# Optimization experiments

Measured on AMD Instinct MI355X. Metric: run time of the kernel, lower is better.

The kernel has to match this reference:

```python
import jax, jax.numpy as jnp
import numpy as np

GAMMA = 5.0 / 3.0
SG = float(np.sqrt(GAMMA - 1.0))
NC, E, H = 1000000, 5, 32

def _csnd(rho, p):
    h = 1.0 + GAMMA / (GAMMA - 1.0) * p / rho
    return jnp.sqrt(GAMMA * p / (rho * h))

def _vstar_from_cs(cs, cs_a, v_a, wave_sign):
    # Marti-Muller relativistic rarefaction Riemann invariant
    ratio = ((SG - cs) / (SG + cs)) * ((SG + cs_a) / (SG - cs_a))
    A = ((1.0 + v_a) / (1.0 - v_a)) * ratio ** (-wave_sign * 2.0 / SG)
    return (A - 1.0) / (A + 1.0)

def _get_vel_raref(p, rho_a, p_a, v_a, wave_sign):
    rho = rho_a * (p / p_a) ** (1.0 / GAMMA)          # isentrope
    h = 1.0 + GAMMA / (GAMMA - 1.0) * p / rho
    cs = jnp.sqrt(GAMMA * p / (rho * h))
    vstar = _vstar_from_cs(cs, _csnd(rho_a, p_a), v_a, wave_sign)
    W = 1.0 / jnp.sqrt(1.0 - vstar ** 2)
    return rho, p / rho, h, cs, vstar, W

def _raref_solver(prims, sign):
    # state inside the rarefaction fan at xi = x/t = 0: v = sign*cs
    rho_a, p_a, v_a = prims[:, 0], prims[:, 1], prims[:, 2]
    cs_a = _csnd(rho_a, p_a)
    wave_sign = -float(sign)
    f = lambda cs: _vstar_from_cs(cs, cs_a, v_a, wave_sign) - sign * cs
    lo = jnp.full_like(rho_a, 1e-6)
    hi = jnp.full_like(rho_a, SG - 1e-6)
    flo = f(lo)
    for _ in range(40):  # fixed-count bisection, jit-safe
        mid = 0.5 * (lo + hi)
        fm = f(mid)
        same = jnp.sign(fm) == jnp.sign(flo)
        lo = jnp.where(same, mid, lo)
        flo = jnp.where(same, fm, flo)
        hi = jnp.where(same, hi, mid)
    cs = 0.5 * (lo + hi)
    h = (GAMMA - 1.0) / (GAMMA - 1.0 - cs ** 2)
    k = (h - 1.0) * (GAMMA - 1.0) / GAMMA              # p / rho
    rho = (k * rho_a ** GAMMA / p_a) ** (1.0 / (GAMMA - 1.0))
    return rho, k * rho, h, sign * cs

def setup_inputs():
    key = jax.random.key(0)
    ks = jax.random.split(key, 10)
    rho = 0.5 + jax.random.uniform(ks[0], (NC, 1, 2))
    p = 0.5 + jax.random.uniform(ks[1], (NC, 1, 2))
    v = 0.8 * (jax.random.uniform(ks[2], (NC, 1, 2)) - 0.5)
    P = jnp.concatenate([rho, p, v], axis=1)           # (NC,3,2)
    U = jax.random.normal(ks[3], (NC, 3, 2))
    F = jax.random.normal(ks[4], (NC, 3, 2))
    cmax = jax.random.uniform(ks[5], (NC,))
    cmin = -jax.random.uniform(ks[6], (NC,))
    s = lambda fan: 0.5 / np.sqrt(fan)
    W1 = jax.random.normal(ks[7], (E, H, 6)) * s(6)
    b1 = jnp.zeros((E, H))
    W2 = jax.random.normal(ks[8], (E, H, H)) * s(H)
    b2 = jnp.zeros((E, H))
    W3 = jax.random.normal(ks[9], (E, 1, H)) * s(H)
    b3 = jnp.zeros((E, 1))
    return {"P": P, "U": U, "F": F, "cmax": cmax, "cmin": cmin,
            "W1": W1, "b1": b1, "W2": W2, "b2": b2, "W3": W3, "b3": b3}

def _forward(P, U, F, cmax, cmin, W1, b1, W2, b2, W3, b3):
    rhoL, rhoR = P[:, 0, 0], P[:, 0, 1]
    pL, pR = P[:, 1, 0], P[:, 1, 1]
    vL, vR = P[:, 2, 0], P[:, 2, 1]
    # pressnet ensemble, batched over E instead of a Python loop
    x = jnp.concatenate([jnp.log(P[:, 0]), jnp.log(P[:, 1]), P[:, 2]], axis=1)  # (NC,6)
    h1 = jnp.tanh(jnp.einsum('nf,ehf->neh', x, W1) + b1)
    h2 = jnp.tanh(jnp.einsum('neh,egh->neg', h1, W2) + b2)
    xi = jax.nn.sigmoid(jnp.einsum('neh,eoh->neo', h2, W3) + b3)[..., 0]        # (NC,E)
    pressC = xi * jnp.minimum(pL, pR)[:, None]        # affine compactification [0, min(pL,pR)]
    rhoCLe, _, hCLe, csCLe, vstarLe, _ = _get_vel_raref(pressC, rhoL[:, None], pL[:, None], vL[:, None], -1.0)
    rhoCRe, _, hCRe, csCRe, vstarRe, _ = _get_vel_raref(pressC, rhoR[:, None], pR[:, None], vR[:, None], +1.0)
    best = jnp.argmin(jnp.abs(vstarLe - vstarRe), axis=1)
    pick = lambda a: jnp.take_along_axis(a, best[:, None], axis=1)[:, 0]
    pressCs = pick(pressC)
    rhoCL, hCL, csCL, vstarL = pick(rhoCLe), pick(hCLe), pick(csCLe), pick(vstarLe)
    rhoCR, hCR, csCR, vstarR = pick(rhoCRe), pick(hCRe), pick(csCRe), pick(vstarRe)
    csL, csR = _csnd(rhoL, pL), _csnd(rhoR, pR)
    lambdaC = 0.5 * (vstarR + vstarL)
    lambdaRL = (lambdaC - csCL) / (1.0 - lambdaC * csCL)
    lambdaL = (vL - csL) / (1.0 - vL * csL)
    lambdaRR = (lambdaC + csCR) / (1.0 + lambdaC * csCR)
    lambdaR = (vR + csR) / (1.0 + vR * csR)
    WC = 1.0 / jnp.sqrt(1.0 - lambdaC ** 2)
    densCL, densCR = WC * rhoCL, WC * rhoCR
    momCL = WC ** 2 * rhoCL * hCL * lambdaC
    momCR = WC ** 2 * rhoCR * hCR * lambdaC
    FCL = jnp.stack([densCL * lambdaC, densCL * (WC * hCL - 1.0) * lambdaC, momCL * lambdaC + pressCs], axis=1)
    FCR = jnp.stack([densCR * lambdaC, densCR * (WC * hCR - 1.0) * lambdaC, momCR * lambdaC + pressCs], axis=1)
    rho_RL, p_RL, h_RL, v_RL = _raref_solver(P[:, :3, 0], +1.0)
    rho_RR, p_RR, h_RR, v_RR = _raref_solver(P[:, :3, 1], -1.0)
    WRL = 1.0 / jnp.sqrt(1.0 - v_RL ** 2)
    WRR = 1.0 / jnp.sqrt(1.0 - v_RR ** 2)
    densRL, densRR = WRL * rho_RL, WRR * rho_RR
    momRL = WRL ** 2 * rho_RL * h_RL * v_RL
    momRR = WRR ** 2 * rho_RR * h_RR * v_RR
    FRL = jnp.stack([densRL * v_RL, densRL * (WRL * h_RL - 1.0) * v_RL, momRL * v_RL + p_RL], axis=1)
    FRR = jnp.stack([densRR * v_RR, densRR * (WRR * h_RR - 1.0) * v_RR, momRR * v_RR + p_RR], axis=1)
    fluxes = jnp.zeros_like(F[:, :, 0])
    sel = lambda m, val, cur: jnp.where(m[:, None], val, cur)
    fluxes = sel(lambdaL >= 0, F[:, :, 0], fluxes)
    fluxes = sel((lambdaL < 0) & (lambdaRL >= 0), FRL, fluxes)
    fluxes = sel((lambdaRL < 0) & (lambdaC > 0), FCL, fluxes)
    fluxes = sel((lambdaC <= 0) & (lambdaRR > 0), FCR, fluxes)
    fluxes = sel((lambdaRR <= 0) & (lambdaR > 0), FRR, fluxes)
    fluxes = sel(lambdaR <= 0, F[:, :, 1], fluxes)
    return fluxes

def reference(P, U, F, cmax, cmin, W1, b1, W2, b2, W3, b3):
    return _forward(P, U, F, cmax, cmin, W1, b1, W2, b2, W3, b3)
```

## Files before the change

kernel.cpp:

```cpp
#include <hip/hip_runtime.h>
#include <hip/hip_bf16.h>
#include <math.h>
#include <stdint.h>

namespace {

constexpr int NE  = 5;
constexpr int NH  = 32;
constexpr int BLK = 256;
constexpr int WPB = BLK / 64;

typedef __attribute__((ext_vector_type(8))) _Float16 half8;
typedef __attribute__((ext_vector_type(2))) __fp16   fp16x2;
typedef __attribute__((ext_vector_type(4))) float    f32x4;

union U4H8 { uint4 u; half8 h; };
union U1H2 { uint32_t u; fp16x2 h; };

__device__ __forceinline__ float bflo(uint32_t u){ return __uint_as_float(u << 16); }
__device__ __forceinline__ float bfhi(uint32_t u){ return __uint_as_float(u & 0xffff0000u); }
__device__ __forceinline__ float b2f(uint16_t u){ return __uint_as_float(((uint32_t)u) << 16); }

constexpr float GAM   = (float)(5.0 / 3.0);
constexpr float G1    = (float)(2.0 / 3.0);
constexpr float CP    = 2.5f;
constexpr float SGc   = (float)0.81649658092772603;
constexpr float E2SG  = (float)2.4494897427831781;
constexpr float LOG2E = 1.4426950408889634f;
constexpr float LN2   = 0.6931471805599453f;
constexpr float TLG   = 2.0f * LOG2E;

__device__ __forceinline__ float fexp2(float x){ return __builtin_amdgcn_exp2f(x); }
__device__ __forceinline__ float flog2(float x){ return __builtin_amdgcn_logf(x); }
__device__ __forceinline__ float frcp (float x){ return __builtin_amdgcn_rcpf(x); }
__device__ __forceinline__ float frsq (float x){ return __builtin_amdgcn_rsqf(x); }
__device__ __forceinline__ float fdiv (float a, float b){ return a * frcp(b); }

__device__ __forceinline__ float tanh_e(float a){
    float e = fexp2(a);
    return 1.0f - 2.0f * frcp(e + 1.0f);
}

__device__ __forceinline__ float csnd_fast(float rho, float p){
    return sqrtf(GAM * p * frcp(rho + CP * p));
}

__device__ __forceinline__ uint32_t pk16(float a, float b){
    U1H2 x; x.h = __builtin_amdgcn_cvt_pkrtz(a, b); return x.u;
}
__device__ __forceinline__ uint32_t pkrtn(float a, float b){
    union { _Float16 h[2]; uint32_t u; } cv;
    cv.h[0] = (_Float16)a; cv.h[1] = (_Float16)b;
    return cv.u;
}

__device__ __forceinline__ int kxr(int r){ return (r ^ (r >> 2)) & 3; }

template<bool F32>
__device__ __forceinline__ float wload(const void* p, int idx){
    if constexpr (F32) return ((const float*)p)[idx];
    else               return b2f(((const uint16_t*)p)[idx]);
}

struct VelRaref { float por, h, cs, vstar; };

__device__ __forceinline__ VelRaref get_vel_raref(float l2p, float l2pa,
                                                  float l2rhoa, float lnra2, float lnv2, float e){
    VelRaref r;
    r.por = fexp2(0.4f * l2p + 0.6f * l2pa - l2rhoa);
    r.h   = 1.0f + CP * r.por;
    r.cs  = sqrtf(GAM * r.por * frcp(r.h));
    float lr2 = flog2((SGc - r.cs) * frcp(SGc + r.cs));
    float A   = fexp2(lnv2 + e * (lr2 + lnra2));
    r.vstar = 1.0f - 2.0f * frcp(A + 1.0f);
    return r;
}

__device__ __forceinline__ void raref_solver(float l2rho_a, float p_a, float sgn,
                                             float lnra2, float lnv2,
                                             float& rho, float& p, float& h, float& v){
    float sE = sgn * E2SG;
    float lo = 1e-6f, hi = SGc - 1e-6f;
    float cs = 0.40f;
    #pragma unroll 1
    for(int it = 0; it < 12; ++it){
        float lr2 = flog2((SGc - cs) * frcp(SGc + cs));
        float a2  = flog2((1.0f + cs) * frcp(1.0f - cs));
        float g   = lnv2 + sE * (lr2 + lnra2) - sgn * a2;
        float d1  = (SGc - cs) * (SGc + cs);
        float d2  = (1.0f - cs) * (1.0f + cs);
        float num = LOG2E * (-2.0f * SGc * sE * d2 - 2.0f * sgn * d1);
        float csn = cs - g * d1 * d2 * frcp(num);
        bool above = (g * sgn > 0.0f);
        lo = above ? cs : lo;
        hi = above ? hi : cs;
        csn = (csn > lo && csn < hi) ? csn : 0.5f * (lo + hi);
        cs = csn;
    }
    h = G1 * frcp(G1 - cs * cs);
    float k = (h - 1.0f) * 0.4f;
    float base = k * fexp2(GAM * l2rho_a) * frcp(p_a);
    rho = base * sqrtf(base);
    p = k * rho;
    v = sgn * cs;
}

template<bool F32>
__device__ __forceinline__ void cell_block(const void* Pp, const void* Fp,
                                           const void* W1p, const void* b1p,
                                           const void* W2p, const void* b2p,
                                           const void* W3p, const void* b3p,
                                           float* __restrict__ out, int nc,
                                           uint32_t* Hu ,
                                           uint32_t* sW1u, uint32_t* sW2u,
                                           float* sB1, float* sB2, float* sW3, float* sB3)
{
    const int lane = threadIdx.x & 63;
    const int l16  = lane & 15;
    const int quad = lane >> 4;
    const int k16  = kxr(l16);
    const int sw   = quad ^ k16;

    for(int i = threadIdx.x; i < NE * NH * 16; i += BLK){
        int row = i >> 4, kp = i & 15;
        float f0 = wload<F32>(W2p, row * NH + 2 * kp) * TLG;
        float f1 = wload<F32>(W2p, row * NH + 2 * kp + 1) * TLG;
        int idx = (row << 4) | ((((kp >> 2) ^ kxr(row)) << 2) | (kp & 3));
        sW2u[idx] = pkrtn(f0, f1);
    }
    for(int i = threadIdx.x; i < NE * NH * 16; i += BLK){
        int row = i >> 4, kp = i & 15;
        int k0 = 2 * kp, k1 = 2 * kp + 1;
        float f0 = (k0 < 6) ? wload<F32>(W1p, row * 6 + k0) * ((k0 < 4) ? 2.0f : TLG) : 0.0f;
        float f1 = (k1 < 6) ? wload<F32>(W1p, row * 6 + k1) * ((k1 < 4) ? 2.0f : TLG) : 0.0f;
        int idx = (row << 4) | ((((kp >> 2) ^ kxr(row)) << 2) | (kp & 3));
        sW1u[idx] = pkrtn(f0, f1);
    }
    for(int i = threadIdx.x; i < NE * NH; i += BLK){
        sB1[i] = wload<F32>(b1p, i) * TLG;
        sB2[i] = wload<F32>(b2p, i) * TLG;
        sW3[i] = wload<F32>(W3p, i);
    }
    if(threadIdx.x < NE) sB3[threadIdx.x] = wload<F32>(b3p, threadIdx.x);
    __syncthreads();

    const int n  = blockIdx.x * BLK + threadIdx.x;
    const bool valid = (n < nc);
    const int nn = valid ? n : 0;

    float rhoL, rhoR, pL, pR, vL, vR;
    if constexpr (F32){
        const float2* Pf = (const float2*)((const float*)Pp + (size_t)nn * 6);
        float2 a = Pf[0], b = Pf[1], c = Pf[2];
        rhoL = a.x; rhoR = a.y; pL = b.x; pR = b.y; vL = c.x; vR = c.y;
    } else {
        const uint32_t* P32 = (const uint32_t*)Pp;
        uint32_t pa = P32[nn * 3 + 0], pb = P32[nn * 3 + 1], pc = P32[nn * 3 + 2];
        rhoL = bflo(pa); rhoR = bfhi(pa);
        pL   = bflo(pb); pR   = bfhi(pb);
        vL   = bflo(pc); vR   = bfhi(pc);
    }

    float l2rhoL = flog2(rhoL), l2rhoR = flog2(rhoR);
    float l2pL   = flog2(pL),   l2pR   = flog2(pR);

    float csL = csnd_fast(rhoL, pL);
    float csR = csnd_fast(rhoR, pR);
    float pmin = fminf(pL, pR);

    float lnraL = flog2((SGc + csL) * frcp(SGc - csL));
    float lnraR = flog2((SGc + csR) * frcp(SGc - csR));
    float lnvL  = flog2((1.0f + vL) * frcp(1.0f - vL));
    float lnvR  = flog2((1.0f + vR) * frcp(1.0f - vR));

    uint4 Bx[4];
    {
        uint32_t x01 = pk16(l2rhoL, l2rhoR);
        uint32_t x23 = pk16(l2pL, l2pR);
        uint32_t x45 = pk16(vL, vR);
        uint4 z = make_uint4(0u, 0u, 0u, 0u);
        *(uint4*)&Hu[(lane << 4) + ((0 ^ k16) << 2)] = make_uint4(x01, x23, x45, 0u);
        *(uint4*)&Hu[(lane << 4) + ((1 ^ k16) << 2)] = z;
        *(uint4*)&Hu[(lane << 4) + ((2 ^ k16) << 2)] = z;
        *(uint4*)&Hu[(lane << 4) + ((3 ^ k16) << 2)] = z;
        #pragma unroll
        for(int t = 0; t < 4; ++t)
            Bx[t] = *(const uint4*)&Hu[((t * 16 + l16) << 4) + (sw << 2)];
    }

    float bestd = 1e30f;
    float pressCs = 0.f, porL = 1.f, hCL = 0.f, csCL = 0.f, vstarL = 0.f;
    float porR = 1.f, hCR = 0.f, csCR = 0.f, vstarR = 0.f;

    #pragma unroll 1
    for(int e = 0; e < NE; ++e){
        U4H8 A1[2];
        #pragma unroll
        for(int m2 = 0; m2 < 2; ++m2)
            A1[m2].u = *(const uint4*)&sW1u[((e * NH + m2 * 16 + l16) << 4) + (sw << 2)];

        f32x4 acc1[2][4];
        #pragma unroll
        for(int m2 = 0; m2 < 2; ++m2){
            f32x4 bias = *(const f32x4*)&sB1[e * NH + m2 * 16 + quad * 4];
            #pragma unroll
            for(int t = 0; t < 4; ++t) acc1[m2][t] = bias;
        }
        #pragma unroll
        for(int t = 0; t < 4; ++t){
            U4H8 Bh; Bh.u = Bx[t];
            #pragma unroll
            for(int m2 = 0; m2 < 2; ++m2)
                acc1[m2][t] = __builtin_amdgcn_mfma_f32_16x16x32_f16(A1[m2].h, Bh.h, acc1[m2][t], 0, 0, 0);
        }

        #pragma unroll
        for(int m2 = 0; m2 < 2; ++m2){
            int cpos = (((m2 * 2 + (quad >> 1)) ^ k16) << 2) + ((quad & 1) << 1);
            #pragma unroll
            for(int t = 0; t < 4; ++t){
                int c = t * 16 + l16;
                uint32_t u0 = pk16(tanh_e(acc1[m2][t][0]), tanh_e(acc1[m2][t][1]));
                uint32_t u1 = pk16(tanh_e(acc1[m2][t][2]), tanh_e(acc1[m2][t][3]));
                *(uint2*)&Hu[(c << 4) + cpos] = make_uint2(u0, u1);
            }
        }

        U4H8 Ah[2];
        #pragma unroll
        for(int m2 = 0; m2 < 2; ++m2)
            Ah[m2].u = *(const uint4*)&sW2u[((e * NH + m2 * 16 + l16) << 4) + (sw << 2)];

        f32x4 acc[2][4];
        #pragma unroll
        for(int m2 = 0; m2 < 2; ++m2){
            f32x4 bias = *(const f32x4*)&sB2[e * NH + m2 * 16 + quad * 4];
            #pragma unroll
            for(int t = 0; t < 4; ++t) acc[m2][t] = bias;
        }

        #pragma unroll
        for(int t = 0; t < 4; ++t){
            int cell = t * 16 + l16;
            U4H8 Bh;
            Bh.u = *(const uint4*)&Hu[(cell << 4) + (sw << 2)];
            #pragma unroll
            for(int m2 = 0; m2 < 2; ++m2)
                acc[m2][t] = __builtin_amdgcn_mfma_f32_16x16x32_f16(Ah[m2].h, Bh.h, acc[m2][t], 0, 0, 0);
        }

        f32x4 w3v[2];
        #pragma unroll
        for(int m2 = 0; m2 < 2; ++m2)
            w3v[m2] = *(const f32x4*)&sW3[e * NH + m2 * 16 + quad * 4];
        float part[4];
        #pragma unroll
        for(int t = 0; t < 4; ++t){
            float s = 0.0f;
            #pragma unroll
            for(int m2 = 0; m2 < 2; ++m2)
                #pragma unroll
                for(int r = 0; r < 4; ++r)
                    s += w3v[m2][r] * tanh_e(acc[m2][t][r]);
            s += __shfl_xor(s, 16, 64);
            s += __shfl_xor(s, 32, 64);
            part[t] = s;
        }
        float p01 = (lane & 16) ? part[1] : part[0];
        float p23 = (lane & 16) ? part[3] : part[2];
        float xa  = ((lane & 32) ? p23 : p01) + sB3[e];

        float xi = frcp(1.0f + fexp2(-xa * LOG2E));
        float pC = xi * pmin;

        float l2pC = flog2(pC);
        VelRaref L = get_vel_raref(l2pC, l2pL, l2rhoL, lnraL, lnvL, +E2SG);
        VelRaref R = get_vel_raref(l2pC, l2pR, l2rhoR, lnraR, lnvR, -E2SG);
        float d = fabsf(L.vstar - R.vstar);
        if(d < bestd){
            bestd = d;
            pressCs = pC;
            porL = L.por; hCL = L.h; csCL = L.cs; vstarL = L.vstar;
            porR = R.por; hCR = R.h; csCR = R.cs; vstarR = R.vstar;
        }
    }

    float rhoCL = pressCs * frcp(porL);
    float rhoCR = pressCs * frcp(porR);

    float lambdaC  = 0.5f * (vstarR + vstarL);
    float lambdaRL = fdiv(lambdaC - csCL, 1.0f - lambdaC * csCL);
    float lambdaL  = fdiv(vL - csL,       1.0f - vL * csL);
    float lambdaRR = fdiv(lambdaC + csCR, 1.0f + lambdaC * csCR);
    float lambdaR  = fdiv(vR + csR,       1.0f + vR * csR);

    float WC = frsq(1.0f - lambdaC * lambdaC);
    float densCL = WC * rhoCL, densCR = WC * rhoCR;
    float momCL = WC * WC * rhoCL * hCL * lambdaC;
    float momCR = WC * WC * rhoCR * hCR * lambdaC;
    float FCL0 = densCL * lambdaC;
    float FCL1 = densCL * (WC * hCL - 1.0f) * lambdaC;
    float FCL2 = momCL * lambdaC + pressCs;
    float FCR0 = densCR * lambdaC;
    float FCR1 = densCR * (WC * hCR - 1.0f) * lambdaC;
    float FCR2 = momCR * lambdaC + pressCs;

    float rho_RL, p_RL, h_RL, v_RL;
    raref_solver(l2rhoL, pL, +1.0f, lnraL, lnvL, rho_RL, p_RL, h_RL, v_RL);
    float rho_RR, p_RR, h_RR, v_RR;
    raref_solver(l2rhoR, pR, -1.0f, lnraR, lnvR, rho_RR, p_RR, h_RR, v_RR);

    float WRL = frsq(1.0f - v_RL * v_RL);
    float WRR = frsq(1.0f - v_RR * v_RR);
    float densRL = WRL * rho_RL, densRR = WRR * rho_RR;
    float momRL = WRL * WRL * rho_RL * h_RL * v_RL;
    float momRR = WRR * WRR * rho_RR * h_RR * v_RR;
    float FRL0 = densRL * v_RL;
    float FRL1 = densRL * (WRL * h_RL - 1.0f) * v_RL;
    float FRL2 = momRL * v_RL + p_RL;
    float FRR0 = densRR * v_RR;
    float FRR1 = densRR * (WRR * h_RR - 1.0f) * v_RR;
    float FRR2 = momRR * v_RR + p_RR;

    float FL0, FR0, FL1, FR1, FL2, FR2;
    if constexpr (F32){
        const float2* Ff = (const float2*)((const float*)Fp + (size_t)nn * 6);
        float2 fa = Ff[0], fb = Ff[1], fc = Ff[2];
        FL0 = fa.x; FR0 = fa.y; FL1 = fb.x; FR1 = fb.y; FL2 = fc.x; FR2 = fc.y;
    } else {
        const uint32_t* F32p = (const uint32_t*)Fp;
        uint32_t fa = F32p[nn * 3 + 0], fb = F32p[nn * 3 + 1], fc = F32p[nn * 3 + 2];
        FL0 = bflo(fa); FR0 = bfhi(fa);
        FL1 = bflo(fb); FR1 = bfhi(fb);
        FL2 = bflo(fc); FR2 = bfhi(fc);
    }

    float o0 = 0.f, o1 = 0.f, o2 = 0.f;
    if(lambdaL >= 0.0f)                        { o0 = FL0;  o1 = FL1;  o2 = FL2;  }
    if(lambdaL < 0.0f  && lambdaRL >= 0.0f)    { o0 = FRL0; o1 = FRL1; o2 = FRL2; }
    if(lambdaRL < 0.0f && lambdaC  >  0.0f)    { o0 = FCL0; o1 = FCL1; o2 = FCL2; }
    if(lambdaC  <= 0.0f && lambdaRR >  0.0f)   { o0 = FCR0; o1 = FCR1; o2 = FCR2; }
    if(lambdaRR <= 0.0f && lambdaR  >  0.0f)   { o0 = FRR0; o1 = FRR1; o2 = FRR2; }
    if(lambdaR  <= 0.0f)                       { o0 = FR0;  o1 = FR1;  o2 = FR2;  }

    if(valid){
        out[(size_t)n * 3 + 0] = o0;
        out[(size_t)n * 3 + 1] = o1;
        out[(size_t)n * 3 + 2] = o2;
    }
}

__global__ __launch_bounds__(BLK)
void solver_kernel(const void* __restrict__ Pp,
                   const void* __restrict__ Fp,
                   const void* __restrict__ W1p,
                   const void* __restrict__ b1p,
                   const void* __restrict__ W2p,
                   const void* __restrict__ b2p,
                   const void* __restrict__ W3p,
                   const void* __restrict__ b3p,
                   float* __restrict__ out, int nc)
{
    __shared__ __align__(16) uint32_t HuA[WPB][64 * 16];
    __shared__ __align__(16) uint32_t sW1u[NE * NH * 16];
    __shared__ __align__(16) uint32_t sW2u[NE * NH * 16];
    __shared__ __align__(16) float sB1[NE * NH];
    __shared__ __align__(16) float sB2[NE * NH];
    __shared__ __align__(16) float sW3[NE * NH];
    __shared__ __align__(16) float sB3[NE];
    const int wv = threadIdx.x >> 6;

    const uint32_t* Pd = (const uint32_t*)Pp;
    int votes = 0;
    #pragma unroll
    for(int i = 0; i < 8; ++i){
        float tv = __uint_as_float(Pd[6 * i + 2]);
        votes += (tv >= 0.45f && tv <= 1.55f) ? 1 : 0;
    }
    if(votes >= 4)
        cell_block<true >(Pp, Fp, W1p, b1p, W2p, b2p, W3p, b3p, out, nc,
                          HuA[wv], sW1u, sW2u, sB1, sB2, sW3, sB3);
    else
        cell_block<false>(Pp, Fp, W1p, b1p, W2p, b2p, W3p, b3p, out, nc,
                          HuA[wv], sW1u, sW2u, sB1, sB2, sW3, sB3);
}

}

extern "C" void kernel_launch(void* const* d_in, const int* in_sizes, int n_in,
                              void* d_out, int out_size, void* d_ws, size_t ws_size,
                              hipStream_t stream) {
    const void* P  = d_in[0];
    const void* F  = d_in[2];
    const void* W1 = d_in[5];
    const void* b1 = d_in[6];
    const void* W2 = d_in[7];
    const void* b2 = d_in[8];
    const void* W3 = d_in[9];
    const void* b3 = d_in[10];
    float* out = (float*)d_out;

    int nc = in_sizes[0] / 6;
    dim3 grid((nc + BLK - 1) / BLK);
    hipLaunchKernelGGL(solver_kernel, grid, dim3(BLK), 0, stream,
                       P, F, W1, b1, W2, b2, W3, b3, out, nc);
}
```

Baseline: 233.2 us.

## Batch reciprocals, fold tanh into sigmoid constants, skip unneeded rarefaction solves

Several transcendental reciprocals are merged through a shared-product batch-inverse trick, in tanh evaluation, the vstar computation and the rarefaction solver. The layer-3 tanh is rewritten algebraically so that W3 and b3 fold into precomputed constants. The left and right rarefaction Newton solves are fused into one loop and skipped entirely when no lane in the wave needs them. The W1 shared layout shrinks to only the nonzero K slice, with zeros filled in through lane masking. Batched reciprocals can lose accuracy or overflow when the products grow large.

```diff
diff --git a/kernel.cpp b/kernel.cpp
--- a/kernel.cpp
+++ b/kernel.cpp
@@ -27,7 +27,6 @@
 constexpr float SGc   = (float)0.81649658092772603;
 constexpr float E2SG  = (float)2.4494897427831781;
 constexpr float LOG2E = 1.4426950408889634f;
-constexpr float LN2   = 0.6931471805599453f;
 constexpr float TLG   = 2.0f * LOG2E;
 
 __device__ __forceinline__ float fexp2(float x){ return __builtin_amdgcn_exp2f(x); }
@@ -36,11 +35,6 @@
 __device__ __forceinline__ float frsq (float x){ return __builtin_amdgcn_rsqf(x); }
 __device__ __forceinline__ float fdiv (float a, float b){ return a * frcp(b); }
 
-__device__ __forceinline__ float tanh_e(float a){
-    float e = fexp2(a);
-    return 1.0f - 2.0f * frcp(e + 1.0f);
-}
-
 __device__ __forceinline__ float csnd_fast(float rho, float p){
     return sqrtf(GAM * p * frcp(rho + CP * p));
 }
@@ -62,47 +56,63 @@
     else               return b2f(((const uint16_t*)p)[idx]);
 }
 
-struct VelRaref { float por, h, cs, vstar; };
-
-__device__ __forceinline__ VelRaref get_vel_raref(float l2p, float l2pa,
-                                                  float l2rhoa, float lnra2, float lnv2, float e){
-    VelRaref r;
-    r.por = fexp2(0.4f * l2p + 0.6f * l2pa - l2rhoa);
-    r.h   = 1.0f + CP * r.por;
-    r.cs  = sqrtf(GAM * r.por * frcp(r.h));
-    float lr2 = flog2((SGc - r.cs) * frcp(SGc + r.cs));
-    float A   = fexp2(lnv2 + e * (lr2 + lnra2));
-    r.vstar = 1.0f - 2.0f * frcp(A + 1.0f);
-    return r;
-}
-
-__device__ __forceinline__ void raref_solver(float l2rho_a, float p_a, float sgn,
-                                             float lnra2, float lnv2,
-                                             float& rho, float& p, float& h, float& v){
-    float sE = sgn * E2SG;
-    float lo = 1e-6f, hi = SGc - 1e-6f;
-    float cs = 0.40f;
+__device__ __forceinline__ void binv4(float d0, float d1, float d2, float d3,
+                                      float& i0, float& i1, float& i2, float& i3){
+    float P1 = d0 * d1, P2 = P1 * d2, P3 = P2 * d3;
+    float R3 = frcp(P3);
+    i3 = R3 * P2;
+    float R2 = R3 * d3;
+    i2 = R2 * P1;
+    float R1 = R2 * d2;
+    i1 = R1 * d0;
+    i0 = R1 * d1;
+}
+
+__device__ __forceinline__ void raref_solver2(float l2rhoL_, float pL_, float lnraL, float lnvL,
+                                              float l2rhoR_, float pR_, float lnraR, float lnvR,
+                                              float& rhoRL, float& pRL, float& hRL, float& vRL,
+                                              float& rhoRR, float& pRR, float& hRR, float& vRR)
+{
+    float loL = 1e-6f, hiL = SGc - 1e-6f, csL = 0.40f;
+    float loR = 1e-6f, hiR = SGc - 1e-6f, csR = 0.40f;
     #pragma unroll 1
     for(int it = 0; it < 12; ++it){
-        float lr2 = flog2((SGc - cs) * frcp(SGc + cs));
-        float a2  = flog2((1.0f + cs) * frcp(1.0f - cs));
-        float g   = lnv2 + sE * (lr2 + lnra2) - sgn * a2;
-        float d1  = (SGc - cs) * (SGc + cs);
-        float d2  = (1.0f - cs) * (1.0f + cs);
-        float num = LOG2E * (-2.0f * SGc * sE * d2 - 2.0f * sgn * d1);
-        float csn = cs - g * d1 * d2 * frcp(num);
-        bool above = (g * sgn > 0.0f);
-        lo = above ? cs : lo;
-        hi = above ? hi : cs;
-        csn = (csn > lo && csn < hi) ? csn : 0.5f * (lo + hi);
-        cs = csn;
-    }
-    h = G1 * frcp(G1 - cs * cs);
-    float k = (h - 1.0f) * 0.4f;
-    float base = k * fexp2(GAM * l2rho_a) * frcp(p_a);
-    rho = base * sqrtf(base);
-    p = k * rho;
-    v = sgn * cs;
+        float aL = SGc + csL, aR = SGc + csR;
+        float Pa = aL * aR, Ra = frcp(Pa);
+        float lrL = flog2((SGc - csL) * (Ra * aR));
+        float lrR = flog2((SGc - csR) * (Ra * aL));
+        float bL = 1.0f - csL, bR = 1.0f - csR;
+        float Pb = bL * bR, Rb = frcp(Pb);
+        float a2L = flog2((1.0f + csL) * (Rb * bR));
+        float a2R = flog2((1.0f + csR) * (Rb * bL));
+        float gL = lnvL + E2SG * (lrL + lnraL) - a2L;
+        float gR = lnvR - E2SG * (lrR + lnraR) + a2R;
+        float d1L = (SGc - csL) * aL, d2L = bL * (1.0f + csL);
+        float d1R = (SGc - csR) * aR, d2R = bR * (1.0f + csR);
+        float numL = LOG2E * (-2.0f * SGc * E2SG * d2L - 2.0f * d1L);
+        float numR = LOG2E * ( 2.0f * SGc * E2SG * d2R + 2.0f * d1R);
+        float Pn = numL * numR, Rn = frcp(Pn);
+        float csnL = csL - gL * d1L * d2L * (Rn * numR);
+        float csnR = csR - gR * d1R * d2R * (Rn * numL);
+        bool abL = (gL > 0.0f);
+        bool abR = (gR < 0.0f);
+        loL = abL ? csL : loL;  hiL = abL ? hiL : csL;
+        loR = abR ? csR : loR;  hiR = abR ? hiR : csR;
+        csnL = (csnL > loL && csnL < hiL) ? csnL : 0.5f * (loL + hiL);
+        csnR = (csnR > loR && csnR < hiR) ? csnR : 0.5f * (loR + hiR);
+        csL = csnL; csR = csnR;
+    }
+    float e1L = G1 - csL * csL, e1R = G1 - csR * csR;
+    float Pe = e1L * e1R, Re = frcp(Pe);
+    hRL = G1 * (Re * e1R);  hRR = G1 * (Re * e1L);
+    float kL = (hRL - 1.0f) * 0.4f, kR = (hRR - 1.0f) * 0.4f;
+    float Pp = pL_ * pR_, Rp = frcp(Pp);
+    float baseL = kL * fexp2(GAM * l2rhoL_) * (Rp * pR_);
+    float baseR = kR * fexp2(GAM * l2rhoR_) * (Rp * pL_);
+    rhoRL = baseL * sqrtf(baseL);
+    rhoRR = baseR * sqrtf(baseR);
+    pRL = kL * rhoRL;  pRR = kR * rhoRR;
+    vRL = csL;  vRR = -csR;
 }
 
 template<bool F32>
@@ -112,8 +122,9 @@
                                            const void* W3p, const void* b3p,
                                            float* __restrict__ out, int nc,
                                            uint32_t* Hu ,
-                                           uint32_t* sW1u, uint32_t* sW2u,
-                                           float* sB1, float* sB2, float* sW3, float* sB3)
+                                           uint32_t* sW1u ,
+                                           uint32_t* sW2u ,
+                                           float* sB1, float* sB2, float* sW3, float* sC)
 {
     const int lane = threadIdx.x & 63;
     const int l16  = lane & 15;
@@ -128,20 +139,24 @@
         int idx = (row << 4) | ((((kp >> 2) ^ kxr(row)) << 2) | (kp & 3));
         sW2u[idx] = pkrtn(f0, f1);
     }
-    for(int i = threadIdx.x; i < NE * NH * 16; i += BLK){
-        int row = i >> 4, kp = i & 15;
+    for(int i = threadIdx.x; i < NE * NH * 4; i += BLK){
+        int row = i >> 2, kp = i & 3;
         int k0 = 2 * kp, k1 = 2 * kp + 1;
         float f0 = (k0 < 6) ? wload<F32>(W1p, row * 6 + k0) * ((k0 < 4) ? 2.0f : TLG) : 0.0f;
         float f1 = (k1 < 6) ? wload<F32>(W1p, row * 6 + k1) * ((k1 < 4) ? 2.0f : TLG) : 0.0f;
-        int idx = (row << 4) | ((((kp >> 2) ^ kxr(row)) << 2) | (kp & 3));
-        sW1u[idx] = pkrtn(f0, f1);
+        sW1u[i] = pkrtn(f0, f1);
     }
     for(int i = threadIdx.x; i < NE * NH; i += BLK){
         sB1[i] = wload<F32>(b1p, i) * TLG;
         sB2[i] = wload<F32>(b2p, i) * TLG;
-        sW3[i] = wload<F32>(W3p, i);
-    }
-    if(threadIdx.x < NE) sB3[threadIdx.x] = wload<F32>(b3p, threadIdx.x);
+        sW3[i] = wload<F32>(W3p, i) * (-LOG2E);
+    }
+    if(threadIdx.x < NE){
+        float s = wload<F32>(b3p, threadIdx.x) * (-LOG2E);
+        for(int j = 0; j < NH; ++j)
+            s += wload<F32>(W3p, threadIdx.x * NH + j) * (-LOG2E);
+        sC[threadIdx.x] = s;
+    }
     __syncthreads();
 
     const int n  = blockIdx.x * BLK + threadIdx.x;
@@ -173,19 +188,20 @@
     float lnvL  = flog2((1.0f + vL) * frcp(1.0f - vL));
     float lnvR  = flog2((1.0f + vR) * frcp(1.0f - vR));
 
-    uint4 Bx[4];
+    float c6L = 0.6f * l2pL - l2rhoL;
+    float c6R = 0.6f * l2pR - l2rhoR;
+
+    U4H8 Bx[4];
     {
         uint32_t x01 = pk16(l2rhoL, l2rhoR);
         uint32_t x23 = pk16(l2pL, l2pR);
         uint32_t x45 = pk16(vL, vR);
-        uint4 z = make_uint4(0u, 0u, 0u, 0u);
-        *(uint4*)&Hu[(lane << 4) + ((0 ^ k16) << 2)] = make_uint4(x01, x23, x45, 0u);
-        *(uint4*)&Hu[(lane << 4) + ((1 ^ k16) << 2)] = z;
-        *(uint4*)&Hu[(lane << 4) + ((2 ^ k16) << 2)] = z;
-        *(uint4*)&Hu[(lane << 4) + ((3 ^ k16) << 2)] = z;
-        #pragma unroll
-        for(int t = 0; t < 4; ++t)
-            Bx[t] = *(const uint4*)&Hu[((t * 16 + l16) << 4) + (sw << 2)];
+        *(uint4*)&Hu[(lane << 4) + (k16 << 2)] = make_uint4(x01, x23, x45, 0u);
+        #pragma unroll
+        for(int t = 0; t < 4; ++t){
+            uint4 b = *(const uint4*)&Hu[((t * 16 + l16) << 4) + (kxr(l16) << 2)];
+            Bx[t].u = (quad == 0) ? b : make_uint4(0u, 0u, 0u, 0u);
+        }
     }
 
     float bestd = 1e30f;
@@ -196,8 +212,10 @@
     for(int e = 0; e < NE; ++e){
         U4H8 A1[2];
         #pragma unroll
-        for(int m2 = 0; m2 < 2; ++m2)
-            A1[m2].u = *(const uint4*)&sW1u[((e * NH + m2 * 16 + l16) << 4) + (sw << 2)];
+        for(int m2 = 0; m2 < 2; ++m2){
+            uint4 w = *(const uint4*)&sW1u[(e * NH + m2 * 16 + l16) << 2];
+            A1[m2].u = (quad == 0) ? w : make_uint4(0u, 0u, 0u, 0u);
+        }
 
         f32x4 acc1[2][4];
         #pragma unroll
@@ -207,22 +225,25 @@
             for(int t = 0; t < 4; ++t) acc1[m2][t] = bias;
         }
         #pragma unroll
-        for(int t = 0; t < 4; ++t){
-            U4H8 Bh; Bh.u = Bx[t];
+        for(int t = 0; t < 4; ++t)
             #pragma unroll
             for(int m2 = 0; m2 < 2; ++m2)
-                acc1[m2][t] = __builtin_amdgcn_mfma_f32_16x16x32_f16(A1[m2].h, Bh.h, acc1[m2][t], 0, 0, 0);
-        }
+                acc1[m2][t] = __builtin_amdgcn_mfma_f32_16x16x32_f16(A1[m2].h, Bx[t].h, acc1[m2][t], 0, 0, 0);
 
         #pragma unroll
         for(int m2 = 0; m2 < 2; ++m2){
             int cpos = (((m2 * 2 + (quad >> 1)) ^ k16) << 2) + ((quad & 1) << 1);
             #pragma unroll
             for(int t = 0; t < 4; ++t){
-                int c = t * 16 + l16;
-                uint32_t u0 = pk16(tanh_e(acc1[m2][t][0]), tanh_e(acc1[m2][t][1]));
-                uint32_t u1 = pk16(tanh_e(acc1[m2][t][2]), tanh_e(acc1[m2][t][3]));
-                *(uint2*)&Hu[(c << 4) + cpos] = make_uint2(u0, u1);
+                float d0 = fexp2(acc1[m2][t][0]) + 1.0f;
+                float d1 = fexp2(acc1[m2][t][1]) + 1.0f;
+                float d2 = fexp2(acc1[m2][t][2]) + 1.0f;
+                float d3 = fexp2(acc1[m2][t][3]) + 1.0f;
+                float i0, i1, i2, i3;
+                binv4(d0, d1, d2, d3, i0, i1, i2, i3);
+                uint32_t u0 = pk16(1.0f - 2.0f * i0, 1.0f - 2.0f * i1);
+                uint32_t u1 = pk16(1.0f - 2.0f * i2, 1.0f - 2.0f * i3);
+                *(uint2*)&Hu[((t * 16 + l16) << 4) + cpos] = make_uint2(u0, u1);
             }
         }
 
@@ -258,30 +279,53 @@
         for(int t = 0; t < 4; ++t){
             float s = 0.0f;
             #pragma unroll
-            for(int m2 = 0; m2 < 2; ++m2)
-                #pragma unroll
-                for(int r = 0; r < 4; ++r)
-                    s += w3v[m2][r] * tanh_e(acc[m2][t][r]);
+            for(int m2 = 0; m2 < 2; ++m2){
+                float d0 = fexp2(acc[m2][t][0]) + 1.0f;
+                float d1 = fexp2(acc[m2][t][1]) + 1.0f;
+                float d2 = fexp2(acc[m2][t][2]) + 1.0f;
+                float d3 = fexp2(acc[m2][t][3]) + 1.0f;
+                float i0, i1, i2, i3;
+                binv4(d0, d1, d2, d3, i0, i1, i2, i3);
+                s = fmaf(w3v[m2][0], i0, s);
+                s = fmaf(w3v[m2][1], i1, s);
+                s = fmaf(w3v[m2][2], i2, s);
+                s = fmaf(w3v[m2][3], i3, s);
+            }
             s += __shfl_xor(s, 16, 64);
             s += __shfl_xor(s, 32, 64);
             part[t] = s;
         }
         float p01 = (lane & 16) ? part[1] : part[0];
         float p23 = (lane & 16) ? part[3] : part[2];
-        float xa  = ((lane & 32) ? p23 : p01) + sB3[e];
-
-        float xi = frcp(1.0f + fexp2(-xa * LOG2E));
+        float partS = (lane & 32) ? p23 : p01;
+        float xa = fmaf(-2.0f, partS, sC[e]);
+        float xi = frcp(1.0f + fexp2(xa));
         float pC = xi * pmin;
 
         float l2pC = flog2(pC);
-        VelRaref L = get_vel_raref(l2pC, l2pL, l2rhoL, lnraL, lnvL, +E2SG);
-        VelRaref R = get_vel_raref(l2pC, l2pR, l2rhoR, lnraR, lnvR, -E2SG);
-        float d = fabsf(L.vstar - R.vstar);
+        float porL_ = fexp2(fmaf(0.4f, l2pC, c6L));
+        float porR_ = fexp2(fmaf(0.4f, l2pC, c6R));
+        float hL_ = 1.0f + CP * porL_, hR_ = 1.0f + CP * porR_;
+        float Ph = hL_ * hR_, Rh = frcp(Ph);
+        float csl = sqrtf(GAM * porL_ * (Rh * hR_));
+        float csr = sqrtf(GAM * porR_ * (Rh * hL_));
+        float dl = SGc + csl, dr = SGc + csr;
+        float Pd = dl * dr, Rd = frcp(Pd);
+        float lrl = flog2((SGc - csl) * (Rd * dr));
+        float lrr = flog2((SGc - csr) * (Rd * dl));
+        float AL = fexp2(lnvL + E2SG * (lrl + lnraL));
+        float AR = fexp2(lnvR - E2SG * (lrr + lnraR));
+        float eL = AL + 1.0f, eR = AR + 1.0f;
+        float Pa2 = eL * eR, Ra2 = frcp(Pa2);
+        float vstL = 1.0f - 2.0f * (Ra2 * eR);
+        float vstR = 1.0f - 2.0f * (Ra2 * eL);
+
+        float d = fabsf(vstL - vstR);
         if(d < bestd){
             bestd = d;
             pressCs = pC;
-            porL = L.por; hCL = L.h; csCL = L.cs; vstarL = L.vstar;
-            porR = R.por; hCR = R.h; csCR = R.cs; vstarR = R.vstar;
+            porL = porL_; hCL = hL_; csCL = csl; vstarL = vstL;
+            porR = porR_; hCR = hR_; csCR = csr; vstarR = vstR;
         }
     }
 
@@ -305,10 +349,16 @@
     float FCR1 = densCR * (WC * hCR - 1.0f) * lambdaC;
     float FCR2 = momCR * lambdaC + pressCs;
 
-    float rho_RL, p_RL, h_RL, v_RL;
-    raref_solver(l2rhoL, pL, +1.0f, lnraL, lnvL, rho_RL, p_RL, h_RL, v_RL);
-    float rho_RR, p_RR, h_RR, v_RR;
-    raref_solver(l2rhoR, pR, -1.0f, lnraR, lnvR, rho_RR, p_RR, h_RR, v_RR);
+    float rho_RL = 0.f, p_RL = 0.f, h_RL = 1.f, v_RL = 0.f;
+    float rho_RR = 0.f, p_RR = 0.f, h_RR = 1.f, v_RR = 0.f;
+    bool needL = (lambdaL < 0.0f)  && (lambdaRL >= 0.0f);
+    bool needR = (lambdaRR <= 0.0f) && (lambdaR  >  0.0f);
+    if(__any(needL || needR)){
+        raref_solver2(l2rhoL, pL, lnraL, lnvL,
+                      l2rhoR, pR, lnraR, lnvR,
+                      rho_RL, p_RL, h_RL, v_RL,
+                      rho_RR, p_RR, h_RR, v_RR);
+    }
 
     float WRL = frsq(1.0f - v_RL * v_RL);
     float WRR = frsq(1.0f - v_RR * v_RR);
@@ -362,12 +412,12 @@
                    float* __restrict__ out, int nc)
 {
     __shared__ __align__(16) uint32_t HuA[WPB][64 * 16];
-    __shared__ __align__(16) uint32_t sW1u[NE * NH * 16];
+    __shared__ __align__(16) uint32_t sW1u[NE * NH * 4];
     __shared__ __align__(16) uint32_t sW2u[NE * NH * 16];
     __shared__ __align__(16) float sB1[NE * NH];
     __shared__ __align__(16) float sB2[NE * NH];
     __shared__ __align__(16) float sW3[NE * NH];
-    __shared__ __align__(16) float sB3[NE];
+    __shared__ __align__(16) float sC[NE];
     const int wv = threadIdx.x >> 6;
 
     const uint32_t* Pd = (const uint32_t*)Pp;
@@ -379,10 +429,10 @@
     }
     if(votes >= 4)
         cell_block<true >(Pp, Fp, W1p, b1p, W2p, b2p, W3p, b3p, out, nc,
-                          HuA[wv], sW1u, sW2u, sB1, sB2, sW3, sB3);
+                          HuA[wv], sW1u, sW2u, sB1, sB2, sW3, sC);
     else
         cell_block<false>(Pp, Fp, W1p, b1p, W2p, b2p, W3p, b3p, out, nc,
-                          HuA[wv], sW1u, sW2u, sB1, sB2, sW3, sB3);
+                          HuA[wv], sW1u, sW2u, sB1, sB2, sW3, sC);
 }
 
 }
```

After: 208.4 us. 10.7% less time.
